# Optimization experiments

Hardware: AMD Instinct MI355X
Metric: run time of the kernel (lower is better)

## Reference

```python
import jax, jax.numpy as jnp
import numpy as np
import math

V, L, D, H, S_MAX = 32000, 6, 768, 8, 256
HD = D // H
SCALE_FACTOR = 2  # attn_scale_factor in the original (TUPE-style)
POS_SCALING = float(HD * SCALE_FACTOR) ** (-0.5)
REL_BINS, MAX_DIST = 32, 128


def _rel_pos_bucket_np(rel, num_buckets=REL_BINS, max_distance=MAX_DIST):
    # bidirectional T5-style bucketing (faithful to relative_position_bucket)
    n = -rel
    num_buckets //= 2
    ret = (n < 0).astype(np.int64) * num_buckets
    n = np.abs(n)
    max_exact = num_buckets // 2
    is_small = n < max_exact
    val_if_large = max_exact + (
        np.log(np.maximum(n, 1).astype(np.float32) / max_exact)
        / math.log(max_distance / max_exact) * (num_buckets - max_exact)
    ).astype(np.int64)
    val_if_large = np.minimum(val_if_large, num_buckets - 1)
    ret += np.where(is_small, n, val_if_large)
    return ret


def _layernorm(x, g, b, eps=1e-5):
    mu = jnp.mean(x, axis=-1, keepdims=True)
    var = jnp.var(x, axis=-1, keepdims=True)
    return (x - mu) * jax.lax.rsqrt(var + eps) * g + b


def setup_inputs() -> dict:
    key = jax.random.key(0)
    ks = jax.random.split(key, 16)
    B, S = 32, 256
    init = lambda k, shape: (jax.random.normal(k, shape, jnp.float32) * 0.02)
    pos_idx = np.arange(S)
    rp = _rel_pos_bucket_np(pos_idx[None, :] - pos_idx[:, None])  # [S,S]
    return {
        "tokens": jax.random.randint(ks[0], (B, S), 0, V, dtype=jnp.int32),
        "embed_tokens": init(ks[1], (V, D)),
        "pos_emb": init(ks[2], (S_MAX + 1, D)),
        "pos_q_w": init(ks[3], (D, D)), "pos_q_b": jnp.zeros((D,), jnp.float32),
        "pos_k_w": init(ks[4], (D, D)), "pos_k_b": jnp.zeros((D,), jnp.float32),
        "pos_ln_g": jnp.ones((D,), jnp.float32), "pos_ln_b": jnp.zeros((D,), jnp.float32),
        "rel_bias_table": init(ks[5], (REL_BINS + 1, H)),
        "rp_bucket": jnp.asarray(rp, jnp.int32),
        "Wq": init(ks[6], (L, D, D)), "bq": jnp.zeros((L, D), jnp.float32),
        "Wk": init(ks[7], (L, D, D)), "bk": jnp.zeros((L, D), jnp.float32),
        "Wv": init(ks[8], (L, D, D)), "bv": jnp.zeros((L, D), jnp.float32),
        "Wo": init(ks[9], (L, D, D)), "bo": jnp.zeros((L, D), jnp.float32),
    }


def reference(tokens, embed_tokens, pos_emb, pos_q_w, pos_q_b, pos_k_w, pos_k_b,
              pos_ln_g, pos_ln_b, rel_bias_table, rp_bucket,
              Wq, bq, Wk, bk, Wv, bv, Wo, bo):
    B, S = tokens.shape
    # relative positional bias: bucket lookup -> [H,S,S]
    rel_bias = rel_bias_table[rp_bucket]            # [S,S,H]
    rel_bias = jnp.transpose(rel_bias, (2, 0, 1))   # [H,S,S]
    # absolute positional bias (TUPE): LN(pos) -> per-head q/k -> bmm
    w = _layernorm(pos_emb[:S], pos_ln_g, pos_ln_b)             # [S,D]
    pq = (w @ pos_q_w.T + pos_q_b).reshape(S, H, HD) * POS_SCALING
    pk = (w @ pos_k_w.T + pos_k_b).reshape(S, H, HD)
    abs_bias = jnp.einsum('ihd,jhd->hij', pq, pk)               # [H,S,S]
    bias = (abs_bias + rel_bias)[None]                          # [1,H,S,S]

    x = embed_tokens[tokens]                                    # [B,S,D]
    scale = float(HD * SCALE_FACTOR) ** (-0.5)
    for l in range(L):
        q = (x @ Wq[l].T + bq[l]).reshape(B, S, H, HD) * scale
        k = (x @ Wk[l].T + bk[l]).reshape(B, S, H, HD)
        v = (x @ Wv[l].T + bv[l]).reshape(B, S, H, HD)
        scores = jnp.einsum('bihd,bjhd->bhij', q, k) + bias     # [B,H,S,S]
        attn = jax.nn.softmax(scores, axis=-1)
        o = jnp.einsum('bhij,bjhd->bihd', attn, v).reshape(B, S, D)
        x = o @ Wo[l].T + bo[l]
    return x[:, 0, :]  # sentence rep [B,D]
```

## Files before the change

### kernel.cpp

```cpp
#include <hip/hip_runtime.h>
#include <hip/hip_bf16.h>
#include <math.h>

constexpr int SEQ = 256;
constexpr int DIM = 768;
constexpr int NH  = 8;
constexpr int HD  = 96;

typedef __attribute__((ext_vector_type(8))) short short8;
typedef __attribute__((ext_vector_type(4))) float f32x4;
using bf16 = __hip_bfloat16;

#define ASYNC_COPY16(gptr, lptr) \
  __builtin_amdgcn_global_load_lds((const __attribute__((address_space(1))) void*)(gptr), \
                                   (__attribute__((address_space(3))) void*)(lptr), 16, 0, 0)

__global__ __launch_bounds__(256) void gemm_kernel(
    const float* __restrict__ A, int lda, long aoz,
    const float* __restrict__ W, int ldw, long woz,
    const float* __restrict__ bias, long boz,
    bf16* __restrict__ C, int ldc, long coz,
    int M, int N, int K, float scale,
    const int* __restrict__ rp, const float* __restrict__ rtab)
{
    const int hz = blockIdx.z;
    A += (long)hz * aoz;
    W += (long)hz * woz;
    if (bias) bias += (long)hz * boz;
    C += (long)hz * coz;

    __shared__ float As[16][68];
    __shared__ float Ws[16][68];

    const int bm = blockIdx.y * 64;
    const int bn = blockIdx.x * 64;
    const int tid = threadIdx.x;
    const int tx = tid & 15;
    const int ty = tid >> 4;

    float acc[4][4] = {};

    for (int k0 = 0; k0 < K; k0 += 16) {
#pragma unroll
        for (int i = 0; i < 4; i++) {
            int idx = tid + i * 256;
            int r = idx >> 4, c = idx & 15;
            As[c][r] = A[(long)(bm + r) * lda + (k0 + c)];
            Ws[c][r] = W[(long)(bn + r) * ldw + (k0 + c)];
        }
        __syncthreads();
#pragma unroll
        for (int kk = 0; kk < 16; kk++) {
            const float4 a = *(const float4*)&As[kk][ty * 4];
            const float4 w = *(const float4*)&Ws[kk][tx * 4];
            acc[0][0] += a.x * w.x; acc[0][1] += a.x * w.y; acc[0][2] += a.x * w.z; acc[0][3] += a.x * w.w;
            acc[1][0] += a.y * w.x; acc[1][1] += a.y * w.y; acc[1][2] += a.y * w.z; acc[1][3] += a.y * w.w;
            acc[2][0] += a.z * w.x; acc[2][1] += a.z * w.y; acc[2][2] += a.z * w.z; acc[2][3] += a.z * w.w;
            acc[3][0] += a.w * w.x; acc[3][1] += a.w * w.y; acc[3][2] += a.w * w.z; acc[3][3] += a.w * w.w;
        }
        __syncthreads();
    }

    const int n0 = bn + tx * 4;
    float4 bv = make_float4(0.f, 0.f, 0.f, 0.f);
    if (bias) bv = *(const float4*)&bias[n0];
#pragma unroll
    for (int i = 0; i < 4; i++) {
        const int m = bm + ty * 4 + i;
        float4 r;
        if (rtab) {
            r.x = acc[i][0] * scale + rtab[rp[(n0 + 0) * 256 + m] * 8 + hz];
            r.y = acc[i][1] * scale + rtab[rp[(n0 + 1) * 256 + m] * 8 + hz];
            r.z = acc[i][2] * scale + rtab[rp[(n0 + 2) * 256 + m] * 8 + hz];
            r.w = acc[i][3] * scale + rtab[rp[(n0 + 3) * 256 + m] * 8 + hz];
        } else {
            r.x = (acc[i][0] + bv.x) * scale;
            r.y = (acc[i][1] + bv.y) * scale;
            r.z = (acc[i][2] + bv.z) * scale;
            r.w = (acc[i][3] + bv.w) * scale;
        }
        bf16 t4[4];
        t4[0] = __float2bfloat16(r.x);
        t4[1] = __float2bfloat16(r.y);
        t4[2] = __float2bfloat16(r.z);
        t4[3] = __float2bfloat16(r.w);
        *(uint2*)&C[(long)m * ldc + n0] = *(uint2*)t4;
    }
}

constexpr int RB_A = 10368;
constexpr int RB_B = RB_A + 3456;
constexpr int RB_C = RB_B + 54;
constexpr int RB_D = RB_C + 6144;
constexpr int RB_E = RB_D + 256;
constexpr int RB_F = RB_E + 1152;
constexpr int RB_G = RB_F + 2;

__global__ __launch_bounds__(256) void setup_mega_kernel(
    const int* __restrict__ tokens, const float* __restrict__ embed,
    const float* __restrict__ pos_emb,
    const float* __restrict__ pos_q_w, const float* __restrict__ pos_q_b,
    const float* __restrict__ pos_k_w, const float* __restrict__ pos_k_b,
    const float* __restrict__ pos_ln_g, const float* __restrict__ pos_ln_b,
    const float* __restrict__ Wq, const float* __restrict__ Wk,
    const float* __restrict__ Wv, const float* __restrict__ Wo,
    const float* __restrict__ bq, const float* __restrict__ bk,
    const float* __restrict__ bv,
    bf16* __restrict__ wqkv, bf16* __restrict__ woT, float* __restrict__ bqkv,
    bf16* __restrict__ xb, bf16* __restrict__ wln,
    bf16* __restrict__ wsW, float* __restrict__ wsB, float scale)
{
    const int bid = blockIdx.x, tid = threadIdx.x;

    if (bid < RB_A) {
        const long idx = (long)bid * 256 + tid;
        const long e = idx * 4;
        const int k = (int)(e % 768);
        const long nl = e / 768;
        const int n = (int)(nl % 2304);
        const int l = (int)(nl / 2304);
        const float* src;
        float sc = 1.f;
        if (n < 768)       { src = Wq + ((long)l * 768 + n) * 768; sc = scale; }
        else if (n < 1536) { src = Wk + ((long)l * 768 + (n - 768)) * 768; }
        else               { src = Wv + ((long)l * 768 + (n - 1536)) * 768; }
        const float4 v = *(const float4*)&src[k];
        bf16 tmp[4];
        tmp[0] = __float2bfloat16(v.x * sc);
        tmp[1] = __float2bfloat16(v.y * sc);
        tmp[2] = __float2bfloat16(v.z * sc);
        tmp[3] = __float2bfloat16(v.w * sc);
        *(uint2*)&wqkv[((long)l * 2304 + n) * 768 + k] = *(uint2*)tmp;
    } else if (bid < RB_B) {
        __shared__ float t[32][33];
        const int b2 = bid - RB_A;
        const int l = b2 / 576, r2 = b2 % 576;
        const int c0 = (r2 % 24) * 32, j0 = (r2 / 24) * 32;
        const int tx = tid & 31, ty = tid >> 5;
        const float* src = Wo + (long)l * 768 * 768;
#pragma unroll
        for (int rr = 0; rr < 32; rr += 8)
            t[ty + rr][tx] = src[(long)(c0 + ty + rr) * 768 + j0 + tx];
        __syncthreads();
        bf16* dst = woT + (long)l * 768 * 768;
#pragma unroll
        for (int rr = 0; rr < 32; rr += 8)
            dst[(long)(j0 + ty + rr) * 768 + c0 + tx] = __float2bfloat16(t[tx][ty + rr]);
    } else if (bid < RB_C) {
        const int idx = (bid - RB_B) * 256 + tid;
        if (idx < 6 * 2304) {
            const int n = idx % 2304, l = idx / 2304;
            float v;
            if (n < 768)       v = bq[l * 768 + n] * scale;
            else if (n < 1536) v = bk[l * 768 + (n - 768)];
            else               v = bv[l * 768 + (n - 1536)];
            bqkv[idx] = v;
        }
    } else if (bid < RB_D) {
        const int idx = (bid - RB_C) * 256 + tid;
        const int t = idx / 192;
        const int d = idx - t * 192;
        const int tok = tokens[t];
        const float4 v = ((const float4*)(embed + (long)tok * DIM))[d];
        bf16 tmp[4];
        tmp[0] = __float2bfloat16(v.x);
        tmp[1] = __float2bfloat16(v.y);
        tmp[2] = __float2bfloat16(v.z);
        tmp[3] = __float2bfloat16(v.w);
        *(uint2*)&xb[(long)t * DIM + d * 4] = *(uint2*)tmp;
    } else if (bid < RB_E) {
        __shared__ float buf[256];
        const int i = bid - RB_D;
        const float* row = pos_emb + (long)i * DIM;
        float v0 = row[tid], v1 = row[tid + 256], v2 = row[tid + 512];
        buf[tid] = v0 + v1 + v2;
        __syncthreads();
        for (int off = 128; off > 0; off >>= 1) {
            if (tid < off) buf[tid] += buf[tid + off];
            __syncthreads();
        }
        const float mean = buf[0] * (1.f / 768.f);
        __syncthreads();
        const float d0 = v0 - mean, d1 = v1 - mean, d2 = v2 - mean;
        buf[tid] = d0 * d0 + d1 * d1 + d2 * d2;
        __syncthreads();
        for (int off = 128; off > 0; off >>= 1) {
            if (tid < off) buf[tid] += buf[tid + off];
            __syncthreads();
        }
        const float rstd = rsqrtf(buf[0] * (1.f / 768.f) + 1e-5f);
        bf16* wr = wln + (long)i * DIM;
        wr[tid]       = __float2bfloat16(d0 * rstd * pos_ln_g[tid]       + pos_ln_b[tid]);
        wr[tid + 256] = __float2bfloat16(d1 * rstd * pos_ln_g[tid + 256] + pos_ln_b[tid + 256]);
        wr[tid + 512] = __float2bfloat16(d2 * rstd * pos_ln_g[tid + 512] + pos_ln_b[tid + 512]);
    } else if (bid < RB_F) {
        const long idx = (long)(bid - RB_E) * 256 + tid;
        const long e = idx * 4;
        const float4 v = (e < 589824) ? *(const float4*)&pos_q_w[e]
                                      : *(const float4*)&pos_k_w[e - 589824];
        bf16 tmp[4];
        tmp[0] = __float2bfloat16(v.x);
        tmp[1] = __float2bfloat16(v.y);
        tmp[2] = __float2bfloat16(v.z);
        tmp[3] = __float2bfloat16(v.w);
        *(uint2*)&wsW[e] = *(uint2*)tmp;
    } else {
        const int idx = (bid - RB_F) * 256 + tid;
        wsB[idx] = (idx < 768) ? pos_q_b[idx] : pos_k_b[idx - 768];
    }
}

__global__ __launch_bounds__(256) void fused_bias_kernel(
    const bf16* __restrict__ wqkv, const float* __restrict__ bo,
    const float* __restrict__ bqkv, float* __restrict__ bf_)
{
    const int l = blockIdx.y;
    const int lane = threadIdx.x & 63, wave = threadIdx.x >> 6;
    const int nloc = wave * 8 + (lane >> 3);
    const int seg = lane & 7;
    const int n = blockIdx.x * 32 + nloc;
    const bf16* wrow = wqkv + ((long)(l + 1) * 2304 + n) * 768 + seg * 96;
    const float* bsrc = bo + (long)l * 768 + seg * 96;
    float s = 0.f;
#pragma unroll
    for (int c8 = 0; c8 < 12; c8++) {
        const short8 w8 = *(const short8*)&wrow[c8 * 8];
#pragma unroll
        for (int e = 0; e < 8; e++) {
            bf16 b;
            *(short*)&b = w8[e];
            s += __bfloat162float(b) * bsrc[c8 * 8 + e];
        }
    }
    s += __shfl_xor(s, 1);
    s += __shfl_xor(s, 2);
    s += __shfl_xor(s, 4);
    if (seg == 0) bf_[l * 2304 + n] = s + bqkv[(l + 1) * 2304 + n];
}

#define GEMM_PREF(AS, BS, KB)                                                 \
  {                                                                           \
    _Pragma("unroll")                                                         \
    for (int i = 0; i < 2; i++) {                                             \
      const int u = tid + i * 512;                                            \
      const int r = u >> 3, c = u & 7;                                        \
      const int ca = c ^ (r & 7);                                             \
      ASYNC_COPY16(A + (bm + r) * (long)K + (KB) + ca * 8, &AS[u * 8]);       \
      ASYNC_COPY16(B + (bn + r) * (long)K + (KB) + ca * 8, &BS[u * 8]);       \
    }                                                                         \
  }

#define GEMM_COMPUTE(AS, BS)                                                  \
  {                                                                           \
    _Pragma("unroll")                                                         \
    for (int ks = 0; ks < 2; ks++) {                                          \
      const int cc = ks * 4 + quad;                                           \
      short8 af[4], bfr[2];                                                   \
      _Pragma("unroll")                                                       \
      for (int t = 0; t < 4; t++) {                                           \
        const int ra = wm * 64 + t * 16 + col;                                \
        af[t] = *(const short8*)&AS[ra * 64 + ((cc ^ (ra & 7)) * 8)];         \
      }                                                                       \
      _Pragma("unroll")                                                       \
      for (int t = 0; t < 2; t++) {                                           \
        const int rb = wn * 32 + t * 16 + col;                                \
        bfr[t] = *(const short8*)&BS[rb * 64 + ((cc ^ (rb & 7)) * 8)];        \
      }                                                                       \
      _Pragma("unroll")                                                       \
      for (int tm = 0; tm < 4; tm++)                                          \
        _Pragma("unroll")                                                     \
        for (int tn = 0; tn < 2; tn++)                                        \
          acc[tm][tn] = __builtin_amdgcn_mfma_f32_16x16x32_bf16(af[tm], bfr[tn], acc[tm][tn], 0, 0, 0); \
    }                                                                         \
  }

__global__ __launch_bounds__(512, 4) void gemm_bf16_kernel(
    const bf16* __restrict__ A, const bf16* __restrict__ B,
    const float* __restrict__ bias,
    bf16* __restrict__ Cb, bf16* __restrict__ vTout, float* __restrict__ Cf,
    int N, int K, int swz, long az, long bz, long cz, long biasz, int skipQ)
{
    __shared__ bf16 As0[128 * 64];
    __shared__ bf16 Bs0[128 * 64];
    __shared__ bf16 As1[128 * 64];
    __shared__ bf16 Bs1[128 * 64];

    A += (long)blockIdx.z * az;
    B += (long)blockIdx.z * bz;
    if (Cb) Cb += (long)blockIdx.z * cz;
    if (Cf) Cf += (long)blockIdx.z * cz;
    if (bias) bias += (long)blockIdx.z * biasz;

    const int tid = threadIdx.x;
    const int lane = tid & 63, wave = tid >> 6;
    const int wm = wave & 1, wn = wave >> 1;

    int bmt, bnt;
    if (swz) {
        const int id = blockIdx.x + gridDim.x * blockIdx.y;
        const int xcd = id & 7, loc = id >> 3;
        bmt = xcd * 8 + (loc & 7);
        bnt = loc >> 3;
    } else {
        bmt = blockIdx.y;
        bnt = blockIdx.x;
    }
    if (skipQ && bnt < 6 && (bmt & 1)) return;

    const long bm = (long)bmt * 128, bn = (long)bnt * 128;
    const int col = lane & 15, quad = lane >> 4;

    f32x4 acc[4][2] = {};

    GEMM_PREF(As0, Bs0, 0);
    for (int kk = 0; kk < K; kk += 128) {
        __syncthreads();
        GEMM_PREF(As1, Bs1, kk + 64);
        GEMM_COMPUTE(As0, Bs0);
        __syncthreads();
        if (kk + 128 < K) GEMM_PREF(As0, Bs0, kk + 128);
        GEMM_COMPUTE(As1, Bs1);
    }

    const bool toVT = (vTout != nullptr) && (bn >= 1536);

    if (toVT) {
        __syncthreads();
        bf16* tb = (wave < 4 ? As0 : Bs0) + (wave & 3) * 2048;
#pragma unroll
        for (int tn = 0; tn < 2; tn++) {
            const int nl = tn * 16 + col;
            const float bvv = bias[bn + wn * 32 + nl];
#pragma unroll
            for (int tm = 0; tm < 4; tm++) {
                const int mc = tm * 4 + quad;
                bf16 t4[4];
#pragma unroll
                for (int r = 0; r < 4; r++)
                    t4[r] = __float2bfloat16(acc[tm][tn][r] + bvv);
                *(uint2*)&tb[(nl * 16 + (mc ^ (nl & 15))) * 4] = *(uint2*)t4;
            }
        }
        const int b_  = (int)((bm + wm * 64) >> 8);
        const int s0  = (int)((bm + wm * 64) & 255);
        const long nb = bn + wn * 32 - 1536;
#pragma unroll
        for (int it2 = 0; it2 < 8; it2++) {
            const int nl = it2 * 4 + quad;
            const uint2 v = *(const uint2*)&tb[(nl * 16 + (col ^ (nl & 15))) * 4];
            *(uint2*)&vTout[((long)b_ * 768 + nb + nl) * 256 + s0 + col * 4] = v;
        }
    } else if (Cf) {
#pragma unroll
        for (int tn = 0; tn < 2; tn++) {
            const long n = bn + wn * 32 + tn * 16 + col;
            const float bvv = bias ? bias[n] : 0.f;
#pragma unroll
            for (int tm = 0; tm < 4; tm++) {
                const long m0 = bm + wm * 64 + tm * 16 + quad * 4;
#pragma unroll
                for (int r = 0; r < 4; r++)
                    Cf[(m0 + r) * N + n] = acc[tm][tn][r] + bvv;
            }
        }
    } else {
#pragma unroll
        for (int tn = 0; tn < 2; tn++) {
            const long n = bn + wn * 32 + tn * 16 + col;
            const float bvv = bias ? bias[n] : 0.f;
#pragma unroll
            for (int tm = 0; tm < 4; tm++) {
                const long m0 = bm + wm * 64 + tm * 16 + quad * 4;
#pragma unroll
                for (int r = 0; r < 4; r++)
                    Cb[(m0 + r) * N + n] = __float2bfloat16(acc[tm][tn][r] + bvv);
            }
        }
    }
}

#define PREF_K(DST, JC)                                                      \
  { _Pragma("unroll")                                                        \
    for (int i = 0; i < 4; i++) {                                            \
      const int u = tid + i * 256;                                           \
      const int r = u >> 4, pp = u & 15;                                     \
      const int c = pp ^ (r & 15);                                           \
      ASYNC_COPY16(kbase + ((JC) * 64 + r) * 2304 + c * 8, &DST[u * 8]);     \
    } }

#define PREF_V(DST, KC)                                                      \
  { _Pragma("unroll")                                                        \
    for (int i = 0; i < 3; i++) {                                            \
      const int u = tid + i * 256;                                           \
      const int r = u >> 3, pp = u & 7;                                      \
      const int c = pp ^ (r & 7);                                            \
      ASYNC_COPY16(vbase + r * 256 + (KC) * 64 + c * 8, &DST[u * 8]);        \
    } }

#define SCORE(BUF, JC)                                                       \
  { __builtin_amdgcn_s_setprio(1);                                           \
    _Pragma("unroll")                                                        \
    for (int ks = 0; ks < 3; ks++) {                                         \
      _Pragma("unroll")                                                      \
      for (int jt2 = 0; jt2 < 4; jt2++) {                                    \
        const int row = jt2 * 16 + col;                                      \
        const int c = ks * 4 + quad;                                         \
        const short8 bk_ = *(const short8*)&BUF[row * 128 + ((c ^ (row & 15)) * 8)]; \
        accS[(JC) * 4 + jt2] = __builtin_amdgcn_mfma_f32_16x16x32_bf16(aq[ks], bk_, accS[(JC) * 4 + jt2], 0, 0, 0); \
      } }                                                                     \
    __builtin_amdgcn_s_setprio(0); }

#define PV(BUF, PC)                                                          \
  { __builtin_amdgcn_s_setprio(1);                                           \
    _Pragma("unroll")                                                        \
    for (int k2 = 0; k2 < 2; k2++) {                                         \
      const short8 ap = *(const short8*)&Ps[(wave * 16 + col) * PS + (PC) * 64 + k2 * 32 + quad * 8]; \
      _Pragma("unroll")                                                      \
      for (int nt = 0; nt < 6; nt++) {                                       \
        const int row = nt * 16 + col;                                       \
        const int c = k2 * 4 + quad;                                         \
        const short8 bv_ = *(const short8*)&BUF[row * 64 + ((c ^ (row & 7)) * 8)]; \
        accO[nt] = __builtin_amdgcn_mfma_f32_16x16x32_bf16(ap, bv_, accO[nt], 0, 0, 0); \
      } }                                                                     \
    __builtin_amdgcn_s_setprio(0); }

__global__ __launch_bounds__(256, 3) void attn_mfma_kernel(
    const bf16* __restrict__ qkv, const bf16* __restrict__ vT,
    const bf16* __restrict__ biasT, bf16* __restrict__ o)
{
    constexpr int PS = 136;
    __shared__ bf16 Ps[64 * PS];
    __shared__ bf16 KV0[64 * 128];
    __shared__ bf16 KV1[64 * 128];

    const int blk = blockIdx.x;
    const int h  = blk & 7;
    const int b  = (blk >> 3) & 31;
    const int it = blk >> 8;
    const int i0 = it * 64;
    const int tid = threadIdx.x, lane = tid & 63, wave = tid >> 6;
    const int col = lane & 15, quad = lane >> 4;
    const long rowbase = (long)b * SEQ;

    const bf16* kbase = qkv + rowbase * 2304 + 768 + h * 96;
    const bf16* vbase = vT + ((long)b * 768 + h * 96) * 256;

    PREF_K(KV0, 0);

    short8 aq[3];
    {
        const bf16* qrow = qkv + (rowbase + i0 + wave * 16 + col) * 2304 + h * 96;
#pragma unroll
        for (int ks = 0; ks < 3; ks++)
            aq[ks] = *(const short8*)&qrow[ks * 32 + quad * 8];
    }

    f32x4 accS[16] = {};
    __syncthreads();
    PREF_K(KV1, 1);
    SCORE(KV0, 0);
    __syncthreads();
    PREF_K(KV0, 2);
    SCORE(KV1, 1);
    __syncthreads();
    PREF_K(KV1, 3);
    SCORE(KV0, 2);
    __syncthreads();
    PREF_V(KV0, 0);
    SCORE(KV1, 3);

    const bf16* bbT = biasT + (long)h * SEQ * SEQ + i0 + wave * 16 + quad * 4;
#pragma unroll
    for (int jt = 0; jt < 16; jt++) {
        bf16 b4[4];
        *(uint2*)b4 = *(const uint2*)&bbT[(long)(jt * 16 + col) * SEQ];
        accS[jt][0] += __bfloat162float(b4[0]);
        accS[jt][1] += __bfloat162float(b4[1]);
        accS[jt][2] += __bfloat162float(b4[2]);
        accS[jt][3] += __bfloat162float(b4[3]);
    }

#pragma unroll
    for (int r = 0; r < 4; r++) {
        float t0 = fmaxf(fmaxf(accS[0][r],  accS[1][r]),  accS[2][r]);
        float t1 = fmaxf(fmaxf(accS[3][r],  accS[4][r]),  accS[5][r]);
        float t2 = fmaxf(fmaxf(accS[6][r],  accS[7][r]),  accS[8][r]);
        float t3 = fmaxf(fmaxf(accS[9][r],  accS[10][r]), accS[11][r]);
        float t4 = fmaxf(fmaxf(accS[12][r], accS[13][r]), accS[14][r]);
        float m  = fmaxf(fmaxf(fmaxf(t0, t1), t2), fmaxf(fmaxf(t3, t4), accS[15][r]));
        for (int d = 1; d < 16; d <<= 1) m = fmaxf(m, __shfl_xor(m, d));
        float s = 0.f;
#pragma unroll
        for (int jt = 0; jt < 16; jt++) {
            const float e = __expf(accS[jt][r] - m);
            accS[jt][r] = e;
            s += e;
        }
        for (int d = 1; d < 16; d <<= 1) s += __shfl_xor(s, d);
        const float inv = __builtin_amdgcn_rcpf(s);
#pragma unroll
        for (int jt = 0; jt < 16; jt++) accS[jt][r] *= inv;
        const int prow = wave * 16 + quad * 4 + r;
#pragma unroll
        for (int jt = 0; jt < 8; jt++)
            Ps[prow * PS + jt * 16 + col] = __float2bfloat16(accS[jt][r]);
    }

    f32x4 accO[6] = {};
    __syncthreads();
    PREF_V(KV1, 1);
    PV(KV0, 0);
    __syncthreads();
    PREF_V(KV0, 2);
    PV(KV1, 1);
#pragma unroll
    for (int r = 0; r < 4; r++) {
        const int prow = wave * 16 + quad * 4 + r;
#pragma unroll
        for (int jt = 8; jt < 16; jt++)
            Ps[prow * PS + (jt - 8) * 16 + col] = __float2bfloat16(accS[jt][r]);
    }
    __syncthreads();
    PREF_V(KV1, 3);
    PV(KV0, 0);
    __syncthreads();
    PV(KV1, 1);

#pragma unroll
    for (int nt = 0; nt < 6; nt++)
#pragma unroll
        for (int r = 0; r < 4; r++) {
            const long m = rowbase + i0 + wave * 16 + quad * 4 + r;
            o[m * DIM + h * 96 + nt * 16 + col] = __float2bfloat16(accO[nt][r]);
        }
}

__global__ __launch_bounds__(256) void final_out_kernel(
    const bf16* __restrict__ ob, const float* __restrict__ Wo5,
    const float* __restrict__ bo5, float* __restrict__ out)
{
    __shared__ float os[768];
    const int b = blockIdx.y, ng = blockIdx.x, tid = threadIdx.x;
    const bf16* orow = ob + (long)b * 256 * 768;
    for (int i = tid; i < 768; i += 256) os[i] = __bfloat162float(orow[i]);
    __syncthreads();

    const int n = ng * 32 + (tid >> 3);
    const int seg = tid & 7;
    const float* wrow = Wo5 + (long)n * 768 + seg * 96;
    const float* xs = &os[seg * 96];
    float s = 0.f;
#pragma unroll
    for (int k = 0; k < 96; k += 4) {
        const float4 w = *(const float4*)&wrow[k];
        s += xs[k] * w.x + xs[k + 1] * w.y + xs[k + 2] * w.z + xs[k + 3] * w.w;
    }
    s += __shfl_xor(s, 1);
    s += __shfl_xor(s, 2);
    s += __shfl_xor(s, 4);
    if (seg == 0) out[b * 768 + n] = s + bo5[n];
}

extern "C" void kernel_launch(void* const* d_in, const int* in_sizes, int n_in,
                              void* d_out, int out_size, void* d_ws, size_t ws_size,
                              hipStream_t stream)
{
    const int*   tokens   = (const int*)d_in[0];
    const float* embed    = (const float*)d_in[1];
    const float* pos_emb  = (const float*)d_in[2];
    const float* pos_q_w  = (const float*)d_in[3];
    const float* pos_q_b  = (const float*)d_in[4];
    const float* pos_k_w  = (const float*)d_in[5];
    const float* pos_k_b  = (const float*)d_in[6];
    const float* pos_ln_g = (const float*)d_in[7];
    const float* pos_ln_b = (const float*)d_in[8];
    const float* rel_tab  = (const float*)d_in[9];
    const int*   rp       = (const int*)d_in[10];
    const float* Wq = (const float*)d_in[11];
    const float* bq = (const float*)d_in[12];
    const float* Wk = (const float*)d_in[13];
    const float* bk = (const float*)d_in[14];
    const float* Wv = (const float*)d_in[15];
    const float* bv = (const float*)d_in[16];
    const float* Wo = (const float*)d_in[17];
    const float* bo = (const float*)d_in[18];
    float* out = (float*)d_out;

    char* p = (char*)d_ws;
    auto alloc = [&](size_t bytes) -> char* {
        char* r = p;
        p += (bytes + 255) & ~(size_t)255;
        return r;
    };
    const long NT = 32L * SEQ;

    bf16*  biasT = (bf16*) alloc(8L * SEQ * SEQ * 2);
    bf16*  wlnb  = (bf16*) alloc((long)SEQ * DIM * 2);
    float* pqk   = (float*)alloc(2L * SEQ * DIM * 4);
    bf16*  wsWb  = (bf16*) alloc(2L * 768 * 768 * 2);
    float* wsB   = (float*)alloc(2L * 768 * 4);
    bf16*  xb    = (bf16*) alloc(NT * DIM * 2);
    bf16*  qkv   = (bf16*) alloc(NT * 2304 * 2);
    bf16*  vT    = (bf16*) alloc(NT * DIM * 2);
    bf16*  ob    = (bf16*) alloc(NT * DIM * 2);
    bf16*  wqkv  = (bf16*) alloc(6L * 2304 * 768 * 2);
    bf16*  woT   = (bf16*) alloc(6L * 768 * 768 * 2);
    bf16*  wf    = (bf16*) alloc(5L * 2304 * 768 * 2);
    float* bqkv  = (float*)alloc(6L * 2304 * 4);
    float* bfus  = (float*)alloc(5L * 2304 * 4);

    const float SCALE = 0.07216878364870322f;

    setup_mega_kernel<<<RB_G, 256, 0, stream>>>(
        tokens, embed, pos_emb, pos_q_w, pos_q_b, pos_k_w, pos_k_b,
        pos_ln_g, pos_ln_b, Wq, Wk, Wv, Wo, bq, bk, bv,
        wqkv, woT, bqkv, xb, wlnb, wsWb, wsB, SCALE);

    gemm_bf16_kernel<<<dim3(6, 18, 5), 512, 0, stream>>>(
        wqkv + 2304L * 768, woT, nullptr, wf, nullptr, nullptr, 768, 768, 0,
        2304L * 768, 768L * 768, 2304L * 768, 0, 0);
    fused_bias_kernel<<<dim3(72, 5), 256, 0, stream>>>(wqkv, bo, bqkv, bfus);

    gemm_bf16_kernel<<<dim3(6, 2, 2), 512, 0, stream>>>(
        wlnb, wsWb, wsB, nullptr, nullptr, pqk, 768, 768, 0,
        0, 768L * 768, (long)SEQ * DIM, 768, 0);
    gemm_kernel<<<dim3(4, 4, NH), 256, 0, stream>>>(
        pqk + (long)SEQ * DIM, DIM, HD, pqk, DIM, HD, nullptr, 0,
        biasT, SEQ, (long)SEQ * SEQ, SEQ, SEQ, HD, SCALE, rp, rel_tab);

    gemm_bf16_kernel<<<dim3(18, 64, 1), 512, 0, stream>>>(
        xb, wqkv, bqkv, qkv, vT, nullptr, 2304, 768, 1, 0, 0, 0, 0, 0);
    for (int l = 0; l < 5; l++) {
        attn_mfma_kernel<<<1024, 256, 0, stream>>>(qkv, vT, biasT, ob);
        gemm_bf16_kernel<<<dim3(18, 64, 1), 512, 0, stream>>>(
            ob, wf + (long)l * 2304 * 768, bfus + (long)l * 2304, qkv, vT, nullptr,
            2304, 768, 1, 0, 0, 0, 0, (l == 4) ? 1 : 0);
    }
    attn_mfma_kernel<<<256, 256, 0, stream>>>(qkv, vT, biasT, ob);
    final_out_kernel<<<dim3(24, 32), 256, 0, stream>>>(ob, Wo + 5L * 768 * 768, bo + 5L * 768, out);
}
```

Baseline: 625.8 us.

## Add 256x256-tile QKV GEMM kernel with finer-grained prefetch pipeline

Adds a new GEMM kernel with 256x256 output tiles, 8 waves and double-buffered LDS. Its K-loop is split into half-stage async prefetches interleaved with MFMA bursts, with setprio raised around each burst. It handles the first 2048 output columns, and the remaining 256 columns go to the old 128-tile kernel through a new column-offset parameter. The aim is more data reuse per block and less barrier and latency stall in the per-layer QKV projection. In exchange it adds an extra launch per layer, uses larger register and LDS footprints, and drops the skip of unused Q tiles in the last layer.

```diff
diff --git a/kernel.cpp b/kernel.cpp
--- a/kernel.cpp
+++ b/kernel.cpp
@@ -278,7 +278,7 @@
     const bf16* __restrict__ A, const bf16* __restrict__ B,
     const float* __restrict__ bias,
     bf16* __restrict__ Cb, bf16* __restrict__ vTout, float* __restrict__ Cf,
-    int N, int K, int swz, long az, long bz, long cz, long biasz, int skipQ)
+    int N, int K, int swz, long az, long bz, long cz, long biasz, int nofs, int skipQ)
 {
     __shared__ bf16 As0[128 * 64];
     __shared__ bf16 Bs0[128 * 64];
@@ -322,7 +322,7 @@
         GEMM_COMPUTE(As1, Bs1);
     }
 
-    const bool toVT = (vTout != nullptr) && (bn >= 1536);
+    const bool toVT = (vTout != nullptr) && (bn + nofs >= 1536);
 
     if (toVT) {
         __syncthreads();
@@ -330,7 +330,7 @@
 #pragma unroll
         for (int tn = 0; tn < 2; tn++) {
             const int nl = tn * 16 + col;
-            const float bvv = bias[bn + wn * 32 + nl];
+            const float bvv = bias[nofs + bn + wn * 32 + nl];
 #pragma unroll
             for (int tm = 0; tm < 4; tm++) {
                 const int mc = tm * 4 + quad;
@@ -343,7 +343,7 @@
         }
         const int b_  = (int)((bm + wm * 64) >> 8);
         const int s0  = (int)((bm + wm * 64) & 255);
-        const long nb = bn + wn * 32 - 1536;
+        const long nb = nofs + bn + wn * 32 - 1536;
 #pragma unroll
         for (int it2 = 0; it2 < 8; it2++) {
             const int nl = it2 * 4 + quad;
@@ -374,6 +374,160 @@
 #pragma unroll
                 for (int r = 0; r < 4; r++)
                     Cb[(m0 + r) * N + n] = __float2bfloat16(acc[tm][tn][r] + bvv);
+            }
+        }
+    }
+}
+
+#define STAGE256(matptr, dstTile, kt2, kh)                                    \
+  { const bf16* gsrc = (matptr) + (long)stg_r * 768 + (kt2) * 64 + (kh) * 32 + stg_c * 8; \
+    bf16* ldst = (dstTile) + (kh) * 8192 + stg_u * 8;                         \
+    ASYNC_COPY16(gsrc, ldst);                                                 \
+    ASYNC_COPY16(gsrc + 16 * 768, ldst + 512); }
+
+#define LDA4(buf, ks, mh)                                                     \
+  { _Pragma("unroll")                                                         \
+    for (int t = 0; t < 4; t++) {                                             \
+      const int row = wm * 128 + ((mh) * 4 + t) * 16 + col;                   \
+      af[t] = *(const short8*)&(buf)[(ks) * 8192 + ((row * 32 + quad * 8) ^ ((row & 8) ? 16 : 0))]; } }
+
+#define LDB4(buf, ks)                                                         \
+  { _Pragma("unroll")                                                         \
+    for (int t = 0; t < 4; t++) {                                             \
+      const int row = wn * 64 + t * 16 + col;                                 \
+      bfrag[t] = *(const short8*)&(buf)[(ks) * 8192 + ((row * 32 + quad * 8) ^ ((row & 8) ? 16 : 0))]; } }
+
+#define MM16(mh)                                                              \
+  { __builtin_amdgcn_s_setprio(1);                                            \
+    _Pragma("unroll")                                                         \
+    for (int tm = 0; tm < 4; tm++)                                            \
+      _Pragma("unroll")                                                       \
+      for (int tn = 0; tn < 4; tn++)                                          \
+        acc[(mh) * 4 + tm][tn] = __builtin_amdgcn_mfma_f32_16x16x32_bf16(af[tm], bfrag[tn], acc[(mh) * 4 + tm][tn], 0, 0, 0); \
+    __builtin_amdgcn_s_setprio(0); }
+
+#define BAR() __builtin_amdgcn_s_barrier()
+
+__global__ __launch_bounds__(512, 2) void gemm256_kernel(
+    const bf16* __restrict__ A, const bf16* __restrict__ B,
+    const float* __restrict__ bias, bf16* __restrict__ Cb,
+    bf16* __restrict__ vTout, int N)
+{
+    __shared__ bf16 lds[2][2][16384];
+
+    const int tid = threadIdx.x;
+    const int lane = tid & 63, wave = tid >> 6;
+    const int wm = wave & 1, wn = wave >> 1;
+    const int col = lane & 15, quad = lane >> 4;
+
+    const int id = blockIdx.x;
+    const int bnt = id & 7;
+    const int bmt = id >> 3;
+    const long bm = (long)bmt * 256;
+
+    const bf16* Ab = A + bm * 768;
+    const bf16* Bb = B + (long)bnt * 256 * 768;
+
+    const int stg_u = wave * 128 + lane;
+    const int stg_r = wave * 32 + (lane >> 2);
+    const int stg_c = (lane & 3) ^ ((lane >> 4) & 2);
+
+    bf16* ldsA0 = &lds[0][0][0];
+    bf16* ldsB0 = &lds[0][1][0];
+    bf16* ldsA1 = &lds[1][0][0];
+    bf16* ldsB1 = &lds[1][1][0];
+
+    f32x4 acc[8][4] = {};
+    short8 af[4], bfrag[4];
+
+    STAGE256(Ab, ldsA0, 0, 0);
+    STAGE256(Bb, ldsB0, 0, 0);
+    STAGE256(Ab, ldsA0, 0, 1);
+    STAGE256(Bb, ldsB0, 0, 1);
+    STAGE256(Ab, ldsA1, 1, 0);
+    STAGE256(Bb, ldsB1, 1, 0);
+    asm volatile("s_waitcnt vmcnt(4)" ::: "memory");
+    BAR();
+
+#pragma unroll 2
+    for (int kt = 0; kt < 12; kt++) {
+        bf16* Abuf  = (kt & 1) ? ldsA1 : ldsA0;
+        bf16* Bbuf  = (kt & 1) ? ldsB1 : ldsB0;
+        bf16* AbufN = (kt & 1) ? ldsA0 : ldsA1;
+        bf16* BbufN = (kt & 1) ? ldsB0 : ldsB1;
+
+        LDA4(Abuf, 0, 0);
+        LDB4(Bbuf, 0);
+        if (kt <= 10) STAGE256(Ab, AbufN, kt + 1, 1);
+        BAR();
+        MM16(0);
+
+        LDA4(Abuf, 0, 1);
+        if (kt <= 10) STAGE256(Bb, BbufN, kt + 1, 1);
+        BAR();
+        MM16(1);
+
+        LDA4(Abuf, 1, 0);
+        LDB4(Bbuf, 1);
+        if (kt <= 9) STAGE256(Ab, Abuf, kt + 2, 0);
+        BAR();
+        MM16(0);
+
+        LDA4(Abuf, 1, 1);
+        if (kt <= 9) STAGE256(Bb, Bbuf, kt + 2, 0);
+        if (kt < 10) {
+            asm volatile("s_waitcnt vmcnt(4)" ::: "memory");
+        } else if (kt == 10) {
+            asm volatile("s_waitcnt vmcnt(0)" ::: "memory");
+        }
+        BAR();
+        MM16(1);
+    }
+
+    if (bnt >= 6) {
+        __syncthreads();
+        bf16* tb = &lds[0][0][0] + wave * 2048;
+        const long nbase = (long)bnt * 256 + wn * 64;
+#pragma unroll
+        for (int cm2 = 0; cm2 < 2; cm2++) {
+#pragma unroll
+            for (int cn2 = 0; cn2 < 2; cn2++) {
+#pragma unroll
+                for (int tn = 0; tn < 2; tn++) {
+                    const int nl = tn * 16 + col;
+                    const float bvv = bias[nbase + cn2 * 32 + nl];
+#pragma unroll
+                    for (int tm = 0; tm < 4; tm++) {
+                        const int mc = tm * 4 + quad;
+                        const f32x4 a = acc[cm2 * 4 + tm][cn2 * 2 + tn];
+                        bf16 t4[4];
+#pragma unroll
+                        for (int r = 0; r < 4; r++)
+                            t4[r] = __float2bfloat16(a[r] + bvv);
+                        *(uint2*)&tb[(nl * 16 + (mc ^ (nl & 15))) * 4] = *(uint2*)t4;
+                    }
+                }
+                const int s0 = wm * 128 + cm2 * 64;
+                const long nb = nbase + cn2 * 32 - 1536;
+#pragma unroll
+                for (int it2 = 0; it2 < 8; it2++) {
+                    const int nl = it2 * 4 + quad;
+                    const uint2 v = *(const uint2*)&tb[(nl * 16 + (col ^ (nl & 15))) * 4];
+                    *(uint2*)&vTout[((long)bmt * 768 + nb + nl) * 256 + s0 + col * 4] = v;
+                }
+            }
+        }
+    } else {
+#pragma unroll
+        for (int nf = 0; nf < 4; nf++) {
+            const long n = (long)bnt * 256 + wn * 64 + nf * 16 + col;
+            const float bvv = bias[n];
+#pragma unroll
+            for (int mf = 0; mf < 8; mf++) {
+                const long m0 = bm + wm * 128 + mf * 16 + quad * 4;
+#pragma unroll
+                for (int r = 0; r < 4; r++)
+                    Cb[(m0 + r) * N + n] = __float2bfloat16(acc[mf][nf][r] + bvv);
             }
         }
     }
@@ -618,23 +772,27 @@
 
     gemm_bf16_kernel<<<dim3(6, 18, 5), 512, 0, stream>>>(
         wqkv + 2304L * 768, woT, nullptr, wf, nullptr, nullptr, 768, 768, 0,
-        2304L * 768, 768L * 768, 2304L * 768, 0, 0);
+        2304L * 768, 768L * 768, 2304L * 768, 0, 0, 0);
     fused_bias_kernel<<<dim3(72, 5), 256, 0, stream>>>(wqkv, bo, bqkv, bfus);
 
     gemm_bf16_kernel<<<dim3(6, 2, 2), 512, 0, stream>>>(
         wlnb, wsWb, wsB, nullptr, nullptr, pqk, 768, 768, 0,
-        0, 768L * 768, (long)SEQ * DIM, 768, 0);
+        0, 768L * 768, (long)SEQ * DIM, 768, 0, 0);
     gemm_kernel<<<dim3(4, 4, NH), 256, 0, stream>>>(
         pqk + (long)SEQ * DIM, DIM, HD, pqk, DIM, HD, nullptr, 0,
         biasT, SEQ, (long)SEQ * SEQ, SEQ, SEQ, HD, SCALE, rp, rel_tab);
 
-    gemm_bf16_kernel<<<dim3(18, 64, 1), 512, 0, stream>>>(
-        xb, wqkv, bqkv, qkv, vT, nullptr, 2304, 768, 1, 0, 0, 0, 0, 0);
+    gemm256_kernel<<<256, 512, 0, stream>>>(xb, wqkv, bqkv, qkv, vT, 2304);
+    gemm_bf16_kernel<<<dim3(2, 64, 1), 512, 0, stream>>>(
+        xb, wqkv + 2048L * 768, bqkv, nullptr, vT, nullptr,
+        2304, 768, 0, 0, 0, 0, 0, 2048, 0);
     for (int l = 0; l < 5; l++) {
         attn_mfma_kernel<<<1024, 256, 0, stream>>>(qkv, vT, biasT, ob);
-        gemm_bf16_kernel<<<dim3(18, 64, 1), 512, 0, stream>>>(
-            ob, wf + (long)l * 2304 * 768, bfus + (long)l * 2304, qkv, vT, nullptr,
-            2304, 768, 1, 0, 0, 0, 0, (l == 4) ? 1 : 0);
+        gemm256_kernel<<<256, 512, 0, stream>>>(
+            ob, wf + (long)l * 2304 * 768, bfus + (long)l * 2304, qkv, vT, 2304);
+        gemm_bf16_kernel<<<dim3(2, 64, 1), 512, 0, stream>>>(
+            ob, wf + (long)l * 2304 * 768 + 2048L * 768, bfus + (long)l * 2304,
+            nullptr, vT, nullptr, 2304, 768, 0, 0, 0, 0, 0, 2048, 0);
     }
     attn_mfma_kernel<<<256, 256, 0, stream>>>(qkv, vT, biasT, ob);
     final_out_kernel<<<dim3(24, 32), 256, 0, stream>>>(ob, Wo + 5L * 768 * 768, bo + 5L * 768, out);
```

Measured after the change: 688.0 us. 9.9% more time.
